# Kernel tuning notes

Hardware: AMD Instinct MI355X
Metric: run time of the kernel (lower is better)

## Reference

```python
import jax, jax.numpy as jnp
import numpy as np

EPS = 1e-6

def _complex_linear(xr, xi, wr, wi):
    # torch Linear: y = x @ W.T ; complex: (xr+i*xi)(Wr+i*Wi)
    yr = jnp.einsum('bsd,ed->bse', xr, wr) - jnp.einsum('bsd,ed->bse', xi, wi)
    yi = jnp.einsum('bsd,ed->bse', xr, wi) + jnp.einsum('bsd,ed->bse', xi, wr)
    return yr, yi

def setup_inputs() -> dict:
    key = jax.random.key(0)
    ks = jax.random.split(key, 12)
    B, S, D = 32768, 16, 64
    inp = {
        'z_real': jax.random.normal(ks[0], (B, D), jnp.float32),
        'z_imag': jax.random.normal(ks[1], (B, D), jnp.float32),
        'mem':    jax.random.normal(ks[2], (B, S, 2 * D), jnp.float32),
        'ptr':    jax.random.uniform(ks[3], (B, S), jnp.float32),
        'ctrl':   jax.random.normal(ks[4], (B, 3), jnp.float32),
        'wq_r': jax.random.normal(ks[5], (D, D), jnp.float32) / np.sqrt(D),
        'wq_i': jax.random.normal(ks[6], (D, D), jnp.float32) / np.sqrt(D),
        'wk_r': jax.random.normal(ks[7], (D, D), jnp.float32) / np.sqrt(D),
        'wk_i': jax.random.normal(ks[8], (D, D), jnp.float32) / np.sqrt(D),
        'wv_r': jax.random.normal(ks[9], (D, D), jnp.float32) / np.sqrt(D),
        'wv_i': jax.random.normal(ks[10], (D, D), jnp.float32) / np.sqrt(D),
    }
    return inp

def reference(z_real, z_imag, mem, ptr, ctrl, wq_r, wq_i, wk_r, wk_i, wv_r, wv_i):
    D = z_real.shape[-1]
    # soft push/pop/stay gates, normalized
    g = jax.nn.sigmoid(ctrl)  # (B,3)
    push, pop, stay = g[:, 0:1], g[:, 1:2], g[:, 2:3]
    total = push + pop + stay + EPS
    push, pop, stay = push / total, pop / total, stay / total
    # pointer update via rolls
    ptr_up = jnp.roll(ptr, 1, axis=1)
    ptr_down = jnp.roll(ptr, -1, axis=1)
    new_ptr = push * ptr_up + pop * ptr_down + stay * ptr  # (B,S)
    # memory write
    z_flat = jnp.concatenate([z_real, z_imag], axis=-1)  # (B,2D)
    mem_new = mem * (1.0 - push[..., None]) + push[..., None] * z_flat[:, None, :]
    mr, mi = mem_new[..., :D], mem_new[..., D:]  # (B,S,D) complex memory
    # complex attention over stack slots
    qr, qi = _complex_linear(mr, mi, wq_r, wq_i)
    kr, ki = _complex_linear(mr, mi, wk_r, wk_i)
    vr, vi = _complex_linear(mr, mi, wv_r, wv_i)
    q_flat = jnp.concatenate([qr, qi], axis=-1)  # (B,S,2D)
    k_flat = jnp.concatenate([kr, ki], axis=-1)
    scale = D ** (-0.5)
    scores = jnp.einsum('bse,bte->bst', q_flat, k_flat) * scale  # (B,S,S)
    attn = jax.nn.softmax(scores, axis=-1)
    ar = jnp.einsum('bst,btd->bsd', attn, vr)
    ai = jnp.einsum('bst,btd->bsd', attn, vi)
    att_flat = jnp.concatenate([ar, ai], axis=-1)  # (B,S,2D)
    # pointer-weighted read
    read_flat = (att_flat * new_ptr[..., None]).sum(axis=1)  # (B,2D)
    z_read_r, z_read_i = read_flat[:, :D], read_flat[:, D:]
    active_slots = (new_ptr > 0.1).astype(jnp.float32).sum(axis=1).mean()
    return (z_read_r, z_read_i, mem_new, new_ptr, active_slots)
```

## Files before the change

kernel.cpp:

```cpp
#include <hip/hip_runtime.h>


typedef __bf16 bf16x8 __attribute__((ext_vector_type(8)));
typedef float  f32x4  __attribute__((ext_vector_type(4)));

#define B_TOT   32768
#define GRID_WG 1024
#define NWAVES  (GRID_WG * 4)

__device__ __forceinline__ unsigned short f2bf(float x) {
  __bf16 h = (__bf16)x;
  return __builtin_bit_cast(unsigned short, h);
}

__device__ __forceinline__ float sigm(float x) { return 1.0f / (1.0f + expf(-x)); }

__global__ void ems_zero(unsigned int* c) { if (threadIdx.x == 0) *c = 0u; }

__global__ void ems_fin(const unsigned int* __restrict__ c, float* __restrict__ out) {
  if (threadIdx.x == 0) out[0] = (float)(*c) * (1.0f / 32768.0f);
}

__global__ void __launch_bounds__(256, 2)
ems_main(const float* __restrict__ z_real, const float* __restrict__ z_imag,
         const float* __restrict__ mem,    const float* __restrict__ ptrv,
         const float* __restrict__ ctrl,
         const float* __restrict__ wqr, const float* __restrict__ wqi,
         const float* __restrict__ wkr, const float* __restrict__ wki,
         const float* __restrict__ wvr, const float* __restrict__ wvi,
         float* __restrict__ out_zr, float* __restrict__ out_zi,
         float* __restrict__ out_mem, float* __restrict__ out_ptr,
         unsigned int* __restrict__ ws_cnt)
{
  __shared__ __align__(16) unsigned short lds[40960];

  #pragma unroll
  for (int m = 0; m < 6; ++m) {
    const float* wp = (m==0)?wqr:(m==1)?wqi:(m==2)?wkr:(m==3)?wki:(m==4)?wvr:wvi;
    for (int idx = (int)threadIdx.x; idx < 4096; idx += 256) {
      int e = idx >> 6, d = idx & 63;
      lds[m*4096 + e*64 + (((d>>3) ^ (e&7)) << 3) + (d&7)] = f2bf(wp[idx]);
    }
  }
  __syncthreads();

  const int tid  = (int)threadIdx.x;
  const int lane = tid & 63;
  const int wv   = tid >> 6;
  const int c    = lane & 15;
  const int g    = lane >> 4;

  unsigned short* sq = &lds[24576 + wv * 4096];
  unsigned short* sk = sq + 2048;

  const float4* mem4 = (const float4*)mem;
  const float4* zr4  = (const float4*)z_real;
  const float4* zi4  = (const float4*)z_imag;
  float4* omem4 = (float4*)out_mem;

  float4 cm[8], cz[8], nm[8], nz[8];

  auto loadB = [&](int bb, float4* m4, float4* z4) {
    #pragma unroll
    for (int t4 = 0; t4 < 4; ++t4) {
      int i4 = bb*512 + c*32 + t4*8 + g*2;
      m4[2*t4]   = mem4[i4];
      m4[2*t4+1] = mem4[i4+1];
    }
    int zb = bb*16 + g*2;
    z4[0] = zr4[zb];   z4[1] = zr4[zb+1];
    z4[2] = zr4[zb+8]; z4[3] = zr4[zb+9];
    z4[4] = zi4[zb];   z4[5] = zi4[zb+1];
    z4[6] = zi4[zb+8]; z4[7] = zi4[zb+9];
  };

  unsigned int active_acc = 0u;
  int b = (int)blockIdx.x * 4 + wv;
  if (b < B_TOT) loadB(b, cm, cz);

  bf16x8 zfrag;
  #pragma unroll
  for (int j = 0; j < 8; ++j) zfrag[j] = (__bf16)0.0f;

  while (b < B_TOT) {
    int nb = b + NWAVES;

    float pu = sigm(ctrl[b*3+0]);
    float po = sigm(ctrl[b*3+1]);
    float st = sigm(ctrl[b*3+2]);
    float tot = pu + po + st + 1e-6f;
    pu /= tot; po /= tot; st /= tot;

    float pm = ptrv[b*16 + ((c+15)&15)];
    float pp = ptrv[b*16 + ((c+ 1)&15)];
    float pc = ptrv[b*16 + c];
    float np = pu*pm + po*pp + st*pc;
    if (g == 0) out_ptr[b*16 + c] = np;
    unsigned long long ball = __ballot(np > 0.1f);
    active_acc += (unsigned int)__popcll(ball & 0xFFFFull);

    float wrow[4];
    #pragma unroll
    for (int i = 0; i < 4; ++i) wrow[i] = __shfl(np, g*4 + i, 64);

    float omp = 1.0f - pu;
    bf16x8 af[4], afn[2];
    #pragma unroll
    for (int t4 = 0; t4 < 4; ++t4) {
      float4 a0 = cm[2*t4], a1 = cm[2*t4+1];
      float4 z0 = cz[2*t4], z1 = cz[2*t4+1];
      float4 r0, r1;
      r0.x = a0.x*omp + pu*z0.x;  r0.y = a0.y*omp + pu*z0.y;
      r0.z = a0.z*omp + pu*z0.z;  r0.w = a0.w*omp + pu*z0.w;
      r1.x = a1.x*omp + pu*z1.x;  r1.y = a1.y*omp + pu*z1.y;
      r1.z = a1.z*omp + pu*z1.z;  r1.w = a1.w*omp + pu*z1.w;
      int i4 = b*512 + c*32 + t4*8 + g*2;
      omem4[i4]   = r0;
      omem4[i4+1] = r1;
      af[t4][0]=(__bf16)r0.x; af[t4][1]=(__bf16)r0.y; af[t4][2]=(__bf16)r0.z; af[t4][3]=(__bf16)r0.w;
      af[t4][4]=(__bf16)r1.x; af[t4][5]=(__bf16)r1.y; af[t4][6]=(__bf16)r1.z; af[t4][7]=(__bf16)r1.w;
      if (t4 >= 2) {
        afn[t4-2][0]=(__bf16)(-r0.x); afn[t4-2][1]=(__bf16)(-r0.y);
        afn[t4-2][2]=(__bf16)(-r0.z); afn[t4-2][3]=(__bf16)(-r0.w);
        afn[t4-2][4]=(__bf16)(-r1.x); afn[t4-2][5]=(__bf16)(-r1.y);
        afn[t4-2][6]=(__bf16)(-r1.z); afn[t4-2][7]=(__bf16)(-r1.w);
      }
    }

    if (nb < B_TOT) loadB(nb, nm, nz);

    auto proj = [&](int matr, int mati, int n, f32x4& ar, f32x4& ai) {
      int e  = n*16 + c;
      int eb = e*64;
      int e7 = e & 7;
      #pragma unroll
      for (int t = 0; t < 2; ++t) {
        int ch = ((t*4 + g) ^ e7) << 3;
        bf16x8 fr = *(const bf16x8*)&lds[matr*4096 + eb + ch];
        bf16x8 fi = *(const bf16x8*)&lds[mati*4096 + eb + ch];
        ar = __builtin_amdgcn_mfma_f32_16x16x32_bf16(af[t],   fr, ar, 0,0,0);
        ai = __builtin_amdgcn_mfma_f32_16x16x32_bf16(af[t],   fi, ai, 0,0,0);
        ar = __builtin_amdgcn_mfma_f32_16x16x32_bf16(afn[t],  fi, ar, 0,0,0);
        ai = __builtin_amdgcn_mfma_f32_16x16x32_bf16(af[t+2], fr, ai, 0,0,0);
      }
    };

    #pragma unroll
    for (int n = 0; n < 4; ++n) {
      f32x4 ar = {0.f,0.f,0.f,0.f}, ai = {0.f,0.f,0.f,0.f};
      proj(0, 1, n, ar, ai);
      #pragma unroll
      for (int i = 0; i < 4; ++i) {
        int r = g*4 + i;
        sq[r*128 + (((n*2 + (c>>3)) ^ r) << 3) + (c&7)]     = f2bf(ar[i]);
        sq[r*128 + (((8 + n*2 + (c>>3)) ^ r) << 3) + (c&7)] = f2bf(ai[i]);
      }
    }
    #pragma unroll
    for (int n = 0; n < 4; ++n) {
      f32x4 ar = {0.f,0.f,0.f,0.f}, ai = {0.f,0.f,0.f,0.f};
      proj(2, 3, n, ar, ai);
      #pragma unroll
      for (int i = 0; i < 4; ++i) {
        int r = g*4 + i;
        sk[r*128 + (((n*2 + (c>>3)) ^ r) << 3) + (c&7)]     = f2bf(ar[i]);
        sk[r*128 + (((8 + n*2 + (c>>3)) ^ r) << 3) + (c&7)] = f2bf(ai[i]);
      }
    }

    f32x4 sc = {0.f,0.f,0.f,0.f};
    #pragma unroll
    for (int t = 0; t < 4; ++t) {
      int ch = ((t*4 + g) ^ c) << 3;
      bf16x8 aq = *(const bf16x8*)&sq[c*128 + ch];
      bf16x8 bk = *(const bf16x8*)&sk[c*128 + ch];
      sc = __builtin_amdgcn_mfma_f32_16x16x32_bf16(aq, bk, sc, 0,0,0);
    }
    float a4[4];
    #pragma unroll
    for (int i = 0; i < 4; ++i) {
      float s0 = sc[i] * 0.125f;
      float mx = s0;
      mx = fmaxf(mx, __shfl_xor(mx, 1, 64));
      mx = fmaxf(mx, __shfl_xor(mx, 2, 64));
      mx = fmaxf(mx, __shfl_xor(mx, 4, 64));
      mx = fmaxf(mx, __shfl_xor(mx, 8, 64));
      float ex = expf(s0 - mx);
      float sm = ex;
      sm += __shfl_xor(sm, 1, 64);
      sm += __shfl_xor(sm, 2, 64);
      sm += __shfl_xor(sm, 4, 64);
      sm += __shfl_xor(sm, 8, 64);
      a4[i] = ex / sm;
    }

    #pragma unroll
    for (int n = 0; n < 4; ++n) {
      f32x4 ar = {0.f,0.f,0.f,0.f}, ai = {0.f,0.f,0.f,0.f};
      proj(4, 5, n, ar, ai);
      uint2 prk, pik;
      prk.x = (unsigned)f2bf(ar[0]) | ((unsigned)f2bf(ar[1]) << 16);
      prk.y = (unsigned)f2bf(ar[2]) | ((unsigned)f2bf(ar[3]) << 16);
      pik.x = (unsigned)f2bf(ai[0]) | ((unsigned)f2bf(ai[1]) << 16);
      pik.y = (unsigned)f2bf(ai[2]) | ((unsigned)f2bf(ai[3]) << 16);
      *(uint2*)&sq[(n*16 + c)*16 + g*4]      = prk;
      *(uint2*)&sq[(64 + n*16 + c)*16 + g*4] = pik;
    }

    #pragma unroll
    for (int i = 0; i < 4; ++i) sk[(g*4+i)*16 + c] = f2bf(a4[i]);

    bf16x8 pa = zfrag;
    if (g < 2) pa = *(const bf16x8*)&sk[c*16 + g*8];
    f32x4 o[8];
    #pragma unroll
    for (int n2 = 0; n2 < 8; ++n2) {
      bf16x8 bv = zfrag;
      if (g < 2) bv = *(const bf16x8*)&sq[(n2*16 + c)*16 + g*8];
      f32x4 zz = {0.f,0.f,0.f,0.f};
      o[n2] = __builtin_amdgcn_mfma_f32_16x16x32_bf16(pa, bv, zz, 0,0,0);
    }

    #pragma unroll
    for (int n2 = 0; n2 < 8; ++n2) {
      float pr = o[n2][0]*wrow[0] + o[n2][1]*wrow[1] + o[n2][2]*wrow[2] + o[n2][3]*wrow[3];
      pr += __shfl_xor(pr, 16, 64);
      pr += __shfl_xor(pr, 32, 64);
      if (g == 0 && n2 < 4)  out_zr[b*64 + n2*16 + c] = pr;
      if (g == 1 && n2 >= 4) out_zi[b*64 + (n2-4)*16 + c] = pr;
    }

    #pragma unroll
    for (int j = 0; j < 8; ++j) { cm[j] = nm[j]; cz[j] = nz[j]; }
    b = nb;
  }

  if (lane == 0) atomicAdd(ws_cnt, active_acc);
}

extern "C" void kernel_launch(void* const* d_in, const int* in_sizes, int n_in,
                              void* d_out, int out_size, void* d_ws, size_t ws_size,
                              hipStream_t stream) {
  const float* z_real = (const float*)d_in[0];
  const float* z_imag = (const float*)d_in[1];
  const float* memp   = (const float*)d_in[2];
  const float* ptrv   = (const float*)d_in[3];
  const float* ctrl   = (const float*)d_in[4];
  const float* wq_r   = (const float*)d_in[5];
  const float* wq_i   = (const float*)d_in[6];
  const float* wk_r   = (const float*)d_in[7];
  const float* wk_i   = (const float*)d_in[8];
  const float* wv_r   = (const float*)d_in[9];
  const float* wv_i   = (const float*)d_in[10];

  float* out     = (float*)d_out;
  float* out_zr  = out;
  float* out_zi  = out + 2097152;
  float* out_mem = out + 4194304;
  float* out_ptr = out + 71303168;
  float* out_sc  = out + 71827456;

  unsigned int* cnt = (unsigned int*)d_ws;

  ems_zero<<<1, 64, 0, stream>>>(cnt);
  ems_main<<<GRID_WG, 256, 0, stream>>>(z_real, z_imag, memp, ptrv, ctrl,
                                        wq_r, wq_i, wk_r, wk_i, wv_r, wv_i,
                                        out_zr, out_zi, out_mem, out_ptr, cnt);
  ems_fin<<<1, 64, 0, stream>>>(cnt, out_sc);
}
```

Baseline: 173.7 us.

## Fold Q and K projections into one precomputed matrix and reassociate pointer-weighted read

A new pre-kernel computes M = Wq_flat^T * Wk_flat as a 128x128 bf16 matrix, so scores become X*M*X^T and the separate Q and K projections are replaced by a single projection. The attention-then-pointer-read is reassociated: pointer weights are folded into the attention weights first, then applied directly to the V projection, which removes the PV matmul and its LDS staging. Block size doubles to 512 threads with 8 batches per wave, and the register prefetch of the next batch is dropped. This trades some numeric change from bf16 rounding of M, plus an extra tiny launch, for fewer MFMAs and less LDS traffic, at the cost of losing the software prefetch overlap.

```diff
diff --git a/kernel.cpp b/kernel.cpp
--- a/kernel.cpp
+++ b/kernel.cpp
@@ -5,14 +5,14 @@
 typedef float  f32x4  __attribute__((ext_vector_type(4)));
 
 #define B_TOT   32768
-#define GRID_WG 1024
-#define NWAVES  (GRID_WG * 4)
+#define GRID_WG 512
+#define NWAVES  4096
+#define BPW     8
 
 __device__ __forceinline__ unsigned short f2bf(float x) {
   __bf16 h = (__bf16)x;
   return __builtin_bit_cast(unsigned short, h);
 }
-
 __device__ __forceinline__ float sigm(float x) { return 1.0f / (1.0f + expf(-x)); }
 
 __global__ void ems_zero(unsigned int* c) { if (threadIdx.x == 0) *c = 0u; }
@@ -21,69 +21,93 @@
   if (threadIdx.x == 0) out[0] = (float)(*c) * (1.0f / 32768.0f);
 }
 
-__global__ void __launch_bounds__(256, 2)
+__global__ void __launch_bounds__(128)
+ems_mt(const float* __restrict__ wqr, const float* __restrict__ wqi,
+       const float* __restrict__ wkr, const float* __restrict__ wki,
+       unsigned short* __restrict__ mt)
+{
+  __shared__ float sK[128];
+  const int e2 = (int)blockIdx.x;
+  const int e  = (int)threadIdx.x;
+  float kv;
+  if (e < 64) kv = (e2 < 64) ? wkr[e*64 + e2]      : -wki[e*64 + (e2-64)];
+  else        kv = (e2 < 64) ? wki[(e-64)*64 + e2] :  wkr[(e-64)*64 + (e2-64)];
+  sK[e] = kv;
+  __syncthreads();
+  float acc = 0.0f;
+  #pragma unroll 8
+  for (int Ep = 0; Ep < 64; ++Ep) {
+    float q = (e < 64) ? wqr[Ep*64 + e] : -wqi[Ep*64 + (e-64)];
+    acc += q * sK[Ep];
+  }
+  #pragma unroll 8
+  for (int Ep = 0; Ep < 64; ++Ep) {
+    float q = (e < 64) ? wqi[Ep*64 + e] : wqr[Ep*64 + (e-64)];
+    acc += q * sK[64 + Ep];
+  }
+  mt[e2*128 + e] = f2bf(acc);
+}
+
+__global__ void __launch_bounds__(512, 4)
 ems_main(const float* __restrict__ z_real, const float* __restrict__ z_imag,
          const float* __restrict__ mem,    const float* __restrict__ ptrv,
          const float* __restrict__ ctrl,
-         const float* __restrict__ wqr, const float* __restrict__ wqi,
-         const float* __restrict__ wkr, const float* __restrict__ wki,
-         const float* __restrict__ wvr, const float* __restrict__ wvi,
+         const float* __restrict__ wvr,    const float* __restrict__ wvi,
+         const unsigned short* __restrict__ mt,
          float* __restrict__ out_zr, float* __restrict__ out_zi,
          float* __restrict__ out_mem, float* __restrict__ out_ptr,
          unsigned int* __restrict__ ws_cnt)
 {
   __shared__ __align__(16) unsigned short lds[40960];
 
+  const int tid = (int)threadIdx.x;
+
+  for (int idx = tid; idx < 16384; idx += 512) {
+    int e2 = idx >> 7, e = idx & 127;
+    lds[(e2 << 7) + ((((e >> 3) ^ (e2 & 15))) << 3) + (e & 7)] = mt[idx];
+  }
   #pragma unroll
-  for (int m = 0; m < 6; ++m) {
-    const float* wp = (m==0)?wqr:(m==1)?wqi:(m==2)?wkr:(m==3)?wki:(m==4)?wvr:wvi;
-    for (int idx = (int)threadIdx.x; idx < 4096; idx += 256) {
+  for (int m = 0; m < 2; ++m) {
+    const float* wp = m ? wvi : wvr;
+    for (int idx = tid; idx < 4096; idx += 512) {
       int e = idx >> 6, d = idx & 63;
-      lds[m*4096 + e*64 + (((d>>3) ^ (e&7)) << 3) + (d&7)] = f2bf(wp[idx]);
+      lds[16384 + (m << 12) + (e << 6) + (((d >> 3) ^ (e & 7)) << 3) + (d & 7)] = f2bf(wp[idx]);
     }
   }
   __syncthreads();
 
-  const int tid  = (int)threadIdx.x;
   const int lane = tid & 63;
   const int wv   = tid >> 6;
   const int c    = lane & 15;
   const int g    = lane >> 4;
 
-  unsigned short* sq = &lds[24576 + wv * 4096];
-  unsigned short* sk = sq + 2048;
+  unsigned short* SY = &lds[24576 + (wv << 11)];
 
   const float4* mem4 = (const float4*)mem;
   const float4* zr4  = (const float4*)z_real;
   const float4* zi4  = (const float4*)z_imag;
   float4* omem4 = (float4*)out_mem;
 
-  float4 cm[8], cz[8], nm[8], nz[8];
-
-  auto loadB = [&](int bb, float4* m4, float4* z4) {
+  unsigned int active_acc = 0u;
+  const int b0 = (int)blockIdx.x * 8 + wv;
+
+  for (int it = 0; it < BPW; ++it) {
+    const int b = b0 + it * NWAVES;
+
+    float4 cm[8], cz[8];
     #pragma unroll
     for (int t4 = 0; t4 < 4; ++t4) {
-      int i4 = bb*512 + c*32 + t4*8 + g*2;
-      m4[2*t4]   = mem4[i4];
-      m4[2*t4+1] = mem4[i4+1];
-    }
-    int zb = bb*16 + g*2;
-    z4[0] = zr4[zb];   z4[1] = zr4[zb+1];
-    z4[2] = zr4[zb+8]; z4[3] = zr4[zb+9];
-    z4[4] = zi4[zb];   z4[5] = zi4[zb+1];
-    z4[6] = zi4[zb+8]; z4[7] = zi4[zb+9];
-  };
-
-  unsigned int active_acc = 0u;
-  int b = (int)blockIdx.x * 4 + wv;
-  if (b < B_TOT) loadB(b, cm, cz);
-
-  bf16x8 zfrag;
-  #pragma unroll
-  for (int j = 0; j < 8; ++j) zfrag[j] = (__bf16)0.0f;
-
-  while (b < B_TOT) {
-    int nb = b + NWAVES;
+      int i4 = b*512 + c*32 + t4*8 + g*2;
+      cm[2*t4]   = mem4[i4];
+      cm[2*t4+1] = mem4[i4+1];
+    }
+    {
+      int zb = b*16 + g*2;
+      cz[0] = zr4[zb];   cz[1] = zr4[zb+1];
+      cz[2] = zr4[zb+8]; cz[3] = zr4[zb+9];
+      cz[4] = zi4[zb];   cz[5] = zi4[zb+1];
+      cz[6] = zi4[zb+8]; cz[7] = zi4[zb+9];
+    }
 
     float pu = sigm(ctrl[b*3+0]);
     float po = sigm(ctrl[b*3+1]);
@@ -98,10 +122,6 @@
     if (g == 0) out_ptr[b*16 + c] = np;
     unsigned long long ball = __ballot(np > 0.1f);
     active_acc += (unsigned int)__popcll(ball & 0xFFFFull);
-
-    float wrow[4];
-    #pragma unroll
-    for (int i = 0; i < 4; ++i) wrow[i] = __shfl(np, g*4 + i, 64);
 
     float omp = 1.0f - pu;
     bf16x8 af[4], afn[2];
@@ -127,54 +147,28 @@
       }
     }
 
-    if (nb < B_TOT) loadB(nb, nm, nz);
-
-    auto proj = [&](int matr, int mati, int n, f32x4& ar, f32x4& ai) {
-      int e  = n*16 + c;
-      int eb = e*64;
-      int e7 = e & 7;
+    #pragma unroll
+    for (int n2 = 0; n2 < 8; ++n2) {
+      int e2 = (n2 << 4) + c;
+      f32x4 acc = {0.f,0.f,0.f,0.f};
       #pragma unroll
-      for (int t = 0; t < 2; ++t) {
-        int ch = ((t*4 + g) ^ e7) << 3;
-        bf16x8 fr = *(const bf16x8*)&lds[matr*4096 + eb + ch];
-        bf16x8 fi = *(const bf16x8*)&lds[mati*4096 + eb + ch];
-        ar = __builtin_amdgcn_mfma_f32_16x16x32_bf16(af[t],   fr, ar, 0,0,0);
-        ai = __builtin_amdgcn_mfma_f32_16x16x32_bf16(af[t],   fi, ai, 0,0,0);
-        ar = __builtin_amdgcn_mfma_f32_16x16x32_bf16(afn[t],  fi, ar, 0,0,0);
-        ai = __builtin_amdgcn_mfma_f32_16x16x32_bf16(af[t+2], fr, ai, 0,0,0);
-      }
-    };
-
-    #pragma unroll
-    for (int n = 0; n < 4; ++n) {
-      f32x4 ar = {0.f,0.f,0.f,0.f}, ai = {0.f,0.f,0.f,0.f};
-      proj(0, 1, n, ar, ai);
+      for (int t = 0; t < 4; ++t) {
+        bf16x8 bm = *(const bf16x8*)&lds[(e2 << 7) + ((((t << 2) + g) ^ c) << 3)];
+        acc = __builtin_amdgcn_mfma_f32_16x16x32_bf16(af[t], bm, acc, 0, 0, 0);
+      }
+      int chb = (n2 << 1) | (c >> 3);
       #pragma unroll
       for (int i = 0; i < 4; ++i) {
-        int r = g*4 + i;
-        sq[r*128 + (((n*2 + (c>>3)) ^ r) << 3) + (c&7)]     = f2bf(ar[i]);
-        sq[r*128 + (((8 + n*2 + (c>>3)) ^ r) << 3) + (c&7)] = f2bf(ai[i]);
-      }
-    }
-    #pragma unroll
-    for (int n = 0; n < 4; ++n) {
-      f32x4 ar = {0.f,0.f,0.f,0.f}, ai = {0.f,0.f,0.f,0.f};
-      proj(2, 3, n, ar, ai);
-      #pragma unroll
-      for (int i = 0; i < 4; ++i) {
-        int r = g*4 + i;
-        sk[r*128 + (((n*2 + (c>>3)) ^ r) << 3) + (c&7)]     = f2bf(ar[i]);
-        sk[r*128 + (((8 + n*2 + (c>>3)) ^ r) << 3) + (c&7)] = f2bf(ai[i]);
+        int s = (g << 2) + i;
+        SY[(s << 7) + ((chb ^ s) << 3) + (c & 7)] = f2bf(acc[i]);
       }
     }
 
     f32x4 sc = {0.f,0.f,0.f,0.f};
     #pragma unroll
     for (int t = 0; t < 4; ++t) {
-      int ch = ((t*4 + g) ^ c) << 3;
-      bf16x8 aq = *(const bf16x8*)&sq[c*128 + ch];
-      bf16x8 bk = *(const bf16x8*)&sk[c*128 + ch];
-      sc = __builtin_amdgcn_mfma_f32_16x16x32_bf16(aq, bk, sc, 0,0,0);
+      bf16x8 aq = *(const bf16x8*)&SY[(c << 7) + ((((t << 2) + g) ^ c) << 3)];
+      sc = __builtin_amdgcn_mfma_f32_16x16x32_bf16(aq, af[t], sc, 0, 0, 0);
     }
     float a4[4];
     #pragma unroll
@@ -194,45 +188,41 @@
       a4[i] = ex / sm;
     }
 
+    float npi[4];
+    #pragma unroll
+    for (int i = 0; i < 4; ++i) npi[i] = __shfl(np, (g << 2) + i, 64);
+    float pw = a4[0]*npi[0] + a4[1]*npi[1] + a4[2]*npi[2] + a4[3]*npi[3];
+    pw += __shfl_xor(pw, 16, 64);
+    pw += __shfl_xor(pw, 32, 64);
+    float w4[4];
+    #pragma unroll
+    for (int i = 0; i < 4; ++i) w4[i] = __shfl(pw, (g << 2) + i, 64);
+
     #pragma unroll
     for (int n = 0; n < 4; ++n) {
+      int e = (n << 4) + c, e7 = e & 7, eb = 16384 + (e << 6);
       f32x4 ar = {0.f,0.f,0.f,0.f}, ai = {0.f,0.f,0.f,0.f};
-      proj(4, 5, n, ar, ai);
-      uint2 prk, pik;
-      prk.x = (unsigned)f2bf(ar[0]) | ((unsigned)f2bf(ar[1]) << 16);
-      prk.y = (unsigned)f2bf(ar[2]) | ((unsigned)f2bf(ar[3]) << 16);
-      pik.x = (unsigned)f2bf(ai[0]) | ((unsigned)f2bf(ai[1]) << 16);
-      pik.y = (unsigned)f2bf(ai[2]) | ((unsigned)f2bf(ai[3]) << 16);
-      *(uint2*)&sq[(n*16 + c)*16 + g*4]      = prk;
-      *(uint2*)&sq[(64 + n*16 + c)*16 + g*4] = pik;
-    }
-
-    #pragma unroll
-    for (int i = 0; i < 4; ++i) sk[(g*4+i)*16 + c] = f2bf(a4[i]);
-
-    bf16x8 pa = zfrag;
-    if (g < 2) pa = *(const bf16x8*)&sk[c*16 + g*8];
-    f32x4 o[8];
-    #pragma unroll
-    for (int n2 = 0; n2 < 8; ++n2) {
-      bf16x8 bv = zfrag;
-      if (g < 2) bv = *(const bf16x8*)&sq[(n2*16 + c)*16 + g*8];
-      f32x4 zz = {0.f,0.f,0.f,0.f};
-      o[n2] = __builtin_amdgcn_mfma_f32_16x16x32_bf16(pa, bv, zz, 0,0,0);
-    }
-
-    #pragma unroll
-    for (int n2 = 0; n2 < 8; ++n2) {
-      float pr = o[n2][0]*wrow[0] + o[n2][1]*wrow[1] + o[n2][2]*wrow[2] + o[n2][3]*wrow[3];
-      pr += __shfl_xor(pr, 16, 64);
-      pr += __shfl_xor(pr, 32, 64);
-      if (g == 0 && n2 < 4)  out_zr[b*64 + n2*16 + c] = pr;
-      if (g == 1 && n2 >= 4) out_zi[b*64 + (n2-4)*16 + c] = pr;
-    }
-
-    #pragma unroll
-    for (int j = 0; j < 8; ++j) { cm[j] = nm[j]; cz[j] = nz[j]; }
-    b = nb;
+      #pragma unroll
+      for (int t = 0; t < 2; ++t) {
+        int ch = (((t << 2) + g) ^ e7) << 3;
+        bf16x8 fr = *(const bf16x8*)&lds[eb + ch];
+        bf16x8 fi = *(const bf16x8*)&lds[eb + 4096 + ch];
+        ar = __builtin_amdgcn_mfma_f32_16x16x32_bf16(af[t],   fr, ar, 0,0,0);
+        ai = __builtin_amdgcn_mfma_f32_16x16x32_bf16(af[t],   fi, ai, 0,0,0);
+        ar = __builtin_amdgcn_mfma_f32_16x16x32_bf16(afn[t],  fi, ar, 0,0,0);
+        ai = __builtin_amdgcn_mfma_f32_16x16x32_bf16(af[t+2], fr, ai, 0,0,0);
+      }
+      float prr = ar[0]*w4[0] + ar[1]*w4[1] + ar[2]*w4[2] + ar[3]*w4[3];
+      float pri = ai[0]*w4[0] + ai[1]*w4[1] + ai[2]*w4[2] + ai[3]*w4[3];
+      prr += __shfl_xor(prr, 16, 64);
+      prr += __shfl_xor(prr, 32, 64);
+      pri += __shfl_xor(pri, 16, 64);
+      pri += __shfl_xor(pri, 32, 64);
+      if (g == 0) {
+        out_zr[b*64 + (n << 4) + c] = prr;
+        out_zi[b*64 + (n << 4) + c] = pri;
+      }
+    }
   }
 
   if (lane == 0) atomicAdd(ws_cnt, active_acc);
@@ -260,11 +250,13 @@
   float* out_ptr = out + 71303168;
   float* out_sc  = out + 71827456;
 
-  unsigned int* cnt = (unsigned int*)d_ws;
+  unsigned int*   cnt = (unsigned int*)d_ws;
+  unsigned short* mt  = (unsigned short*)((char*)d_ws + 1024);
 
   ems_zero<<<1, 64, 0, stream>>>(cnt);
-  ems_main<<<GRID_WG, 256, 0, stream>>>(z_real, z_imag, memp, ptrv, ctrl,
-                                        wq_r, wq_i, wk_r, wk_i, wv_r, wv_i,
+  ems_mt<<<128, 128, 0, stream>>>(wq_r, wq_i, wk_r, wk_i, mt);
+  ems_main<<<GRID_WG, 512, 0, stream>>>(z_real, z_imag, memp, ptrv, ctrl,
+                                        wv_r, wv_i, mt,
                                         out_zr, out_zi, out_mem, out_ptr, cnt);
   ems_fin<<<1, 64, 0, stream>>>(cnt, out_sc);
 }
```

Result: slower. 180.6 us (+4.0%).
